# Kernel optimization log

Hardware: AMD Instinct MI355X
Metric: run time of the kernel (lower is better)

The kernel has to match this reference:

```python
import jax, jax.numpy as jnp
import numpy as np


def _gru_dir(x, Wih, Whh, bih, bhh):
    # x: (B,T,I) -> (B,T,H); torch GRU equations, h0 = 0
    H = Whh.shape[1]
    pre = x @ Wih.T + bih  # (B,T,3H), input projection hoisted out of scan
    def step(h, p):
        gh = h @ Whh.T + bhh
        pr, pz, pn = jnp.split(p, 3, axis=-1)
        gr, gz, gn = jnp.split(gh, 3, axis=-1)
        r = jax.nn.sigmoid(pr + gr)
        z = jax.nn.sigmoid(pz + gz)
        n = jnp.tanh(pn + r * gn)
        h = (1.0 - z) * n + z * h
        return h, h
    h0 = jnp.zeros((x.shape[0], H), x.dtype)
    _, ys = jax.lax.scan(step, h0, jnp.swapaxes(pre, 0, 1))
    return jnp.swapaxes(ys, 0, 1)


def _gru_bidir(x, Wih, Whh, bih, bhh):
    f = _gru_dir(x, Wih[0], Whh[0], bih[0], bhh[0])
    b = _gru_dir(x[:, ::-1], Wih[1], Whh[1], bih[1], bhh[1])[:, ::-1]
    return jnp.concatenate([f, b], axis=-1)


def _forward(inputs, embed, l_Wih, l_Whh, l_bih, l_bhh, r_Wih, r_Whh, r_bih, r_bhh,
             a_Wih, a_Whh, a_bih, a_bhh, Wc1, Wc2, vc, Wb, Wd, vd, Wm, vm, Ws, vs,
             Wp, vp, Wpred):
    x = embed[inputs]  # (B,T,E)
    hl = _gru_bidir(x, l_Wih, l_Whh, l_bih, l_bhh)  # (B,T,2H)
    hr = _gru_bidir(x, r_Wih, r_Whh, r_bih, r_bhh)  # (B,T,2H)
    # co-attention: score[b,i,j] = vc . tanh(Wc1 hl_j + Wc2 hr_i)
    s = jnp.tanh((hl @ Wc1.T)[:, None, :, :] + (hr @ Wc2.T)[:, :, None, :])  # (B,T,T,H)
    ptc = jax.nn.softmax((s @ vc.T)[..., 0], axis=-1) @ hl
    # bilinear: hr (Wb hl)^T
    sjt = jnp.einsum('bid,bjd->bij', hr, hl @ Wb.T)
    ptb = jax.nn.softmax(sjt, axis=-1) @ hl
    # multiplicative: vd . tanh(Wd (hl_j * hr_i))
    p = hl[:, None, :, :] * hr[:, :, None, :]  # (B,T,T,2H)
    ptd = jax.nn.softmax((jnp.tanh(p @ Wd.T) @ vd.T)[..., 0], axis=-1) @ hl
    # subtractive: vm . tanh(Wm (hl_j - hr_i))
    d = hl[:, None, :, :] - hr[:, :, None, :]  # (B,T,T,2H)
    ptm = jax.nn.softmax((jnp.tanh(d @ Wm.T) @ vm.T)[..., 0], axis=-1) @ hl
    # self-attention on hr: vs . tanh(Ws (hr_j * hr_i))
    ss = hr[:, None, :, :] * hr[:, :, None, :]  # (B,T,T,2H)
    pts = jax.nn.softmax((jnp.tanh(ss @ Ws.T) @ vs.T)[..., 0], axis=-1) @ hr
    agg = jnp.concatenate([hr, pts, ptc, ptd, ptb, ptm], axis=-1)  # (B,T,12H)
    ar = _gru_bidir(agg, a_Wih, a_Whh, a_bih, a_bhh)  # (B,T,2H)
    # pooling of hl
    sj = jax.nn.softmax(jnp.swapaxes(jnp.tanh(hl @ Wp.T) @ vp.T, 1, 2), axis=-1)  # (B,1,T)
    rl = sj @ hl  # (B,1,2H)
    # final attention over aggregation
    sj2 = jax.nn.softmax(jnp.swapaxes((ar @ Wc1.T + rl @ Wc2.T) @ vc.T, 1, 2), axis=-1)  # (B,1,T)
    rr = (sj2 @ ar)[:, 0, :]  # (B,2H)
    return jax.nn.sigmoid(rr @ Wpred.T)  # (B,labels)


def setup_inputs() -> dict:
    B, T, V, E, H, L = 4, 256, 30000, 300, 128, 2
    key = jax.random.key(0)
    ks = jax.random.split(key, 40)
    inp = {}
    inp['inputs'] = jax.random.randint(ks[0], (B, T), 0, V)
    inp['embed'] = jax.random.uniform(ks[1], (V, E), jnp.float32, -0.1, 0.1)
    ki = 2
    for name, isz in [('l', E), ('r', E), ('a', 12 * H)]:
        inp[name + '_Wih'] = jax.random.normal(ks[ki], (2, 3 * H, isz), jnp.float32) * 0.05; ki += 1
        inp[name + '_Whh'] = jax.random.normal(ks[ki], (2, 3 * H, H), jnp.float32) * 0.05; ki += 1
        inp[name + '_bih'] = jnp.zeros((2, 3 * H), jnp.float32)
        inp[name + '_bhh'] = jnp.zeros((2, 3 * H), jnp.float32)
    for n, o, i in [('Wc1', H, 2 * H), ('Wc2', H, 2 * H), ('vc', 1, H), ('Wb', 2 * H, 2 * H),
                    ('Wd', H, 2 * H), ('vd', 1, H), ('Wm', H, 2 * H), ('vm', 1, H),
                    ('Ws', H, 2 * H), ('vs', 1, H), ('Wp', H, 2 * H), ('vp', 1, H),
                    ('Wpred', L, 2 * H)]:
        inp[n] = jax.random.normal(ks[ki], (o, i), jnp.float32) * 0.05; ki += 1
    return inp


def reference(inputs, embed, l_Wih, l_Whh, l_bih, l_bhh, r_Wih, r_Whh, r_bih, r_bhh,
              a_Wih, a_Whh, a_bih, a_bhh, Wc1, Wc2, vc, Wb, Wd, vd, Wm, vm, Ws, vs,
              Wp, vp, Wpred):
    return _forward(inputs, embed, l_Wih, l_Whh, l_bih, l_bhh, r_Wih, r_Whh, r_bih,
                    r_bhh, a_Wih, a_Whh, a_bih, a_bhh, Wc1, Wc2, vc, Wb, Wd, vd, Wm,
                    vm, Ws, vs, Wp, vp, Wpred)
```

## Files before the change

### kernel.cpp

```cpp
#include <hip/hip_runtime.h>


#define DEV static __device__ __forceinline__
#define BAR_LGKM() __asm__ volatile("s_waitcnt lgkmcnt(0)\ns_barrier" ::: "memory")

typedef __attribute__((ext_vector_type(4))) float f32x4;
typedef __attribute__((ext_vector_type(8))) short s16x8;
typedef __attribute__((ext_vector_type(4))) unsigned int u32x4;
typedef __attribute__((ext_vector_type(2))) unsigned int u32x2;

constexpr int T = 256, E = 300, EP = 320, H = 128, H2 = 256, H3 = 384, H12 = 1536;
constexpr int M = 1024;
constexpr int STY = 262144;

DEV float b2f(unsigned short h) { return __uint_as_float(((unsigned)h) << 16); }
DEV unsigned short f2b(float f) {
  unsigned u = __float_as_uint(f);
  u += 0x7fff + ((u >> 16) & 1);
  return (unsigned short)(u >> 16);
}
DEV unsigned cvt_pk_bf16(float lo, float hi) {
  unsigned r;
  __asm__("v_cvt_pk_bf16_f32 %0, %1, %2" : "=v"(r) : "v"(lo), "v"(hi));
  return r;
}
DEV float rcp_f(float x) {
  float r;
  __asm__("v_rcp_f32 %0, %1" : "=v"(r) : "v"(x));
  return r;
}
DEV float sigm(float x) { return rcp_f(1.f + __expf(-x)); }
DEV float tanh_f(float x) {
  float e = __expf(2.f * x);
  return __builtin_fmaf(-2.f, rcp_f(e + 1.f), 1.f);
}
DEV float plsel(float x0, float x1) {
  u32x2 r = __builtin_amdgcn_permlane32_swap(
      __float_as_uint(x0), __float_as_uint(x1), false, false);
  return __uint_as_float(r[0]);
}

DEV s16x8 ldfrag(const unsigned short* p) {
  u32x4 v = *(const u32x4*)p;
  return __builtin_bit_cast(s16x8, v);
}
DEV f32x4 mfma16(s16x8 a, s16x8 b, f32x4 c) {
  return __builtin_amdgcn_mfma_f32_16x16x32_bf16(a, b, c, 0, 0, 0);
}


struct StageArgs {
  const float* cs[9]; unsigned short* cd[9]; int cn[9];
  const int* idx; const float* emb; unsigned short* xhi; unsigned short* xlo;
  const float* lW; const float* rW; unsigned short* wpad;
  int bo[12];
};

__global__ void k_stage(StageArgs sa) {
  int blk = blockIdx.x;
  int seg = 0;
  #pragma unroll
  for (int s2 = 1; s2 < 11; ++s2) seg = (blk >= sa.bo[s2]) ? s2 : seg;
  int i = (blk - sa.bo[seg]) * 256 + threadIdx.x;
  if (seg < 9) {
    if (i < sa.cn[seg]) sa.cd[seg][i] = f2b(sa.cs[seg][i]);
    return;
  }
  if (seg == 9) {
    if (i >= M * EP) return;
    int m = i / EP, e = i - m * EP;
    int r = sa.idx[m];
    float v = (e < E) ? sa.emb[(size_t)r * E + e] : 0.f;
    unsigned short hi = f2b(v);
    sa.xhi[i] = hi;
    sa.xlo[i] = f2b(v - b2f(hi));
    return;
  }
  if (i >= 4 * H3 * EP) return;
  int e = i % EP, n = (i / EP) % H3, uu = i / (EP * H3);
  const float* src = (uu < 2 ? sa.lW : sa.rW) + (size_t)((uu & 1) * H3 + n) * E;
  sa.wpad[i] = (e < E) ? f2b(src[e]) : (unsigned short)0;
}


struct GemmDesc {
  const unsigned short* Ahi; const unsigned short* Alo; const unsigned short* W;
  const float* bias; float* Cf; int N; int K; int tr;
};
struct GemmBatch { GemmDesc d[8]; };

__global__ __launch_bounds__(256) void k_gemm(GemmBatch gb) {
  GemmDesc g = gb.d[blockIdx.z];
  int nb = blockIdx.y * 64;
  if (nb >= g.N) return;
  int mb = blockIdx.x * 64;
  int lane = threadIdx.x & 63, w = threadIdx.x >> 6, quad = lane >> 4, l16 = lane & 15;
  int K = g.K;
  const unsigned short* Ahp = g.Ahi + (size_t)(mb + w * 16 + l16) * K + quad * 8;
  const unsigned short* Alp = g.Alo + (size_t)(mb + w * 16 + l16) * K + quad * 8;
  const unsigned short* Wp = g.W + (size_t)(nb + l16) * K + quad * 8;
  f32x4 acc[4];
  #pragma unroll
  for (int nt = 0; nt < 4; ++nt) acc[nt] = f32x4{0.f, 0.f, 0.f, 0.f};
  for (int k = 0; k < K; k += 32) {
    s16x8 ah = ldfrag(Ahp + k);
    s16x8 al = ldfrag(Alp + k);
    #pragma unroll
    for (int nt = 0; nt < 4; ++nt) {
      s16x8 b = ldfrag(Wp + (size_t)nt * 16 * K + k);
      acc[nt] = mfma16(ah, b, acc[nt]);
      acc[nt] = mfma16(al, b, acc[nt]);
    }
  }
  int mr0 = mb + w * 16 + quad * 4;
  #pragma unroll
  for (int nt = 0; nt < 4; ++nt) {
    int col = nb + nt * 16 + l16;
    float bv = g.bias ? g.bias[col] : 0.f;
    #pragma unroll
    for (int r = 0; r < 4; ++r) {
      if (g.tr)
        g.Cf[(size_t)col * M + (mr0 + r)] = acc[nt][r] + bv;
      else
        g.Cf[(size_t)(mr0 + r) * g.N + col] = acc[nt][r] + bv;
    }
  }
}


struct RecArgs {
  const unsigned short* whh[4];
  const float* pre[4];
  float* outf[4];
  unsigned short* outhi[4];
  unsigned short* outlo[4];
  unsigned short* agghi[4];
  unsigned short* agglo[4];
  const float* bhh[4];
  int colOff[4];
  int dir[4];
};

#define GRU_STEP(pr_, pz_, pn_, pq_, hcur_, hnxt_, s_)                         \
  {                                                                            \
    float pr = pr_, pz = pz_, pn = pn_;                                        \
    pq_ += pst2;                                                               \
    pr_ = pq_[0] + bh_r; pz_ = pq_[128] + bh_z; pn_ = pq_[256];                \
    const unsigned short* hb_ = hcur_ + l16 * 136 + quad * 8;                  \
    s16x8 ah0 = ldfrag(hb_);                                                   \
    s16x8 ah1 = ldfrag(hb_ + 32);                                              \
    s16x8 ah2 = ldfrag(hb_ + 64);                                              \
    s16x8 ah3 = ldfrag(hb_ + 96);                                              \
    f32x4 z4 = f32x4{0.f, 0.f, 0.f, 0.f};                                      \
    f32x4 aR0 = mfma16(ah0, bq[0][0], z4);                                     \
    f32x4 aR1 = mfma16(ah2, bq[0][2], z4);                                     \
    aR0 = mfma16(ah1, bq[0][1], aR0);                                          \
    aR1 = mfma16(ah3, bq[0][3], aR1);                                          \
    f32x4 aZ0 = mfma16(ah0, bq[1][0], z4);                                     \
    f32x4 aZ1 = mfma16(ah2, bq[1][2], z4);                                     \
    aZ0 = mfma16(ah1, bq[1][1], aZ0);                                          \
    aZ1 = mfma16(ah3, bq[1][3], aZ1);                                          \
    float r0 = (aR0[0] + aR1[0]) + (aR0[1] + aR1[1]);                          \
    float r1v = (aR0[2] + aR1[2]) + (aR0[3] + aR1[3]);                         \
    float rg = sigm(pr + plsel(r0, r1v));                                      \
    f32x4 aN0 = mfma16(ah0, bq[2][0], z4);                                     \
    f32x4 aN1 = mfma16(ah2, bq[2][2], z4);                                     \
    aN0 = mfma16(ah1, bq[2][1], aN0);                                          \
    aN1 = mfma16(ah3, bq[2][3], aN1);                                          \
    float z0 = (aZ0[0] + aZ1[0]) + (aZ0[1] + aZ1[1]);                          \
    float z1 = (aZ0[2] + aZ1[2]) + (aZ0[3] + aZ1[3]);                          \
    float zg = sigm(pz + plsel(z0, z1));                                       \
    float n0 = (aN0[0] + aN1[0]) + (aN0[1] + aN1[1]);                          \
    float n1 = (aN0[2] + aN1[2]) + (aN0[3] + aN1[3]);                          \
    float ng = tanh_f(pn + rg * (plsel(n0, n1) + bh_n));                       \
    hf = __builtin_fmaf(zg, hf - ng, ng);                                      \
    unsigned hp32 = cvt_pk_bf16(hf, hf);                                       \
    float rem = hf - __uint_as_float(hp32 << 16);                              \
    unsigned lp32 = cvt_pk_bf16(rem, rem);                                     \
    unsigned short hi = (unsigned short)hp32;                                  \
    unsigned short lo = (unsigned short)lp32;                                  \
    hnxt_[(2 * b) * 136 + d] = hi;                                             \
    hnxt_[(2 * b + 1) * 136 + d] = lo;                                         \
    int tq = dir ? (T - 1 - (s_)) : (s_);                                      \
    size_t o_ = (size_t)(b * T + tq) * H2 + colOff + d;                        \
    outf[o_] = hf; outhi[o_] = hi; outlo[o_] = lo;                             \
    if (agghi) {                                                               \
      size_t a_ = (size_t)(b * T + tq) * H12 + colOff + d;                     \
      agghi[a_] = hi; agglo[a_] = lo;                                          \
    }                                                                          \
    BAR_LGKM();                                                                \
  }

__global__ __launch_bounds__(512) void k_gru(RecArgs ra) {
  int u = blockIdx.x;
  __shared__ __align__(16) unsigned short hs[2][16 * 136];
  int tid = threadIdx.x, lane = tid & 63, w8 = tid >> 6;
  int quad = lane >> 4, l16 = lane & 15;
  for (int i = tid; i < 2 * 16 * 136; i += 512) ((unsigned short*)hs)[i] = 0;
  const unsigned short* whh = ra.whh[u];
  s16x8 bq[3][4];
  #pragma unroll
  for (int g = 0; g < 3; ++g) {
    int row = g * 128 + w8 * 16 + l16;
    #pragma unroll
    for (int kc = 0; kc < 4; ++kc)
      bq[g][kc] = ldfrag(whh + (size_t)row * H + kc * 32 + quad * 8);
  }
  const float* bhh = ra.bhh[u];
  const float* pre = ra.pre[u];
  float* outf = ra.outf[u];
  unsigned short* outhi = ra.outhi[u];
  unsigned short* outlo = ra.outlo[u];
  unsigned short* agghi = ra.agghi[u];
  unsigned short* agglo = ra.agglo[u];
  int colOff = ra.colOff[u], dir = ra.dir[u];
  int b = ((quad & 1) << 1) | (quad >> 1);
  int d = w8 * 16 + l16;
  float bh_r = bhh[d], bh_z = bhh[d + 128], bh_n = bhh[d + 256];
  float hf = 0.f;
  int t0 = dir ? (T - 1) : 0;
  long pst = dir ? -(long)H3 : (long)H3;
  long pst2 = 2 * pst;
  const float* pqE = pre + (size_t)(b * T + t0) * H3 + d;
  const float* pqO = pqE + pst;
  float e_pr = pqE[0] + bh_r, e_pz = pqE[128] + bh_z, e_pn = pqE[256];
  float o_pr = pqO[0] + bh_r, o_pz = pqO[128] + bh_z, o_pn = pqO[256];
  __syncthreads();
  for (int s = 0; s < T; s += 2) {
    GRU_STEP(e_pr, e_pz, e_pn, pqE, hs[0], hs[1], s);
    GRU_STEP(o_pr, o_pz, o_pn, pqO, hs[1], hs[0], s + 1);
  }
}


struct ScMMArgs {
  const unsigned short* Xhi[2];
  const float* Rf; const float* Wt[2]; const float* vt[2];
  float* So[2]; float* So2[2];
};

__global__ __launch_bounds__(256, 2) void k_scmm(ScMMArgs a) {
  __shared__ __align__(16) unsigned short w_lds[64 * 256];
  int which = blockIdx.y;
  int bi = blockIdx.x, b = bi >> 8;
  int tid = threadIdx.x;
  int type = which >> 1, khb = which & 1;
  const unsigned short* Xhi = a.Xhi[type];
  const float* W = a.Wt[type] + (size_t)khb * 64 * 256;
  const float* v = a.vt[type] + khb * 64;
  float* Sout = khb ? a.So2[type] : a.So[type];
  int lane = tid & 63, w = tid >> 6, quad = lane >> 4, l16 = lane & 15;
  int d4 = tid & 63, rhi = tid >> 6;
  float4 h4 = ((const float4*)(a.Rf + (size_t)bi * 256))[d4];
  #pragma unroll
  for (int it = 0; it < 16; ++it) {
    int kl = it * 4 + rhi;
    float4 w4 = ((const float4*)(W + (size_t)kl * 256))[d4];
    unsigned lo32 = cvt_pk_bf16(w4.x * h4.x, w4.y * h4.y);
    unsigned hi32 = cvt_pk_bf16(w4.z * h4.z, w4.w * h4.w);
    unsigned long long pk = (unsigned long long)lo32 | ((unsigned long long)hi32 << 32);
    int gphys = ((d4 >> 1) + kl) & 31;
    *(unsigned long long*)(w_lds + (size_t)kl * 256 + gphys * 8 + (d4 & 1) * 4) = pk;
  }
  BAR_LGKM();
  f32x4 acc[4][4];
  #pragma unroll
  for (int jj = 0; jj < 4; ++jj)
    #pragma unroll
    for (int c = 0; c < 4; ++c) acc[jj][c] = f32x4{0.f, 0.f, 0.f, 0.f};
  const unsigned short* Xp0 =
      Xhi + (size_t)(b * 256 + w * 4 * 16 + l16) * 256 + quad * 8;
  #pragma unroll 2
  for (int kc = 0; kc < 8; ++kc) {
    s16x8 af[4];
    #pragma unroll
    for (int c = 0; c < 4; ++c) {
      int krow = c * 16 + l16;
      int gp = (kc * 4 + quad + krow) & 31;
      af[c] = ldfrag(w_lds + (size_t)krow * 256 + gp * 8);
    }
    s16x8 bf[4];
    #pragma unroll
    for (int jj = 0; jj < 4; ++jj)
      bf[jj] = ldfrag(Xp0 + (size_t)jj * 16 * 256 + kc * 32);
    #pragma unroll
    for (int jj = 0; jj < 4; ++jj)
      #pragma unroll
      for (int c = 0; c < 4; ++c)
        acc[jj][c] = mfma16(af[c], bf[jj], acc[jj][c]);
  }
  float vv[4][4];
  #pragma unroll
  for (int c = 0; c < 4; ++c)
    #pragma unroll
    for (int r = 0; r < 4; ++r) vv[c][r] = v[c * 16 + quad * 4 + r];
  #pragma unroll
  for (int jj = 0; jj < 4; ++jj) {
    float s = 0.f;
    #pragma unroll
    for (int c = 0; c < 4; ++c)
      #pragma unroll
      for (int r = 0; r < 4; ++r) s += tanh_f(acc[jj][c][r]) * vv[c][r];
    s += __shfl_xor(s, 16);
    s += __shfl_xor(s, 32);
    int jt = w * 4 + jj;
    if (lane < 16) Sout[(size_t)bi * 256 + jt * 16 + l16] = s;
  }
}


struct ScCmbArgs {
  const float *Hc, *Rc, *Hm, *Rm, *HB, *hrf, *vcf, *vmf; float* S;
};

__global__ __launch_bounds__(256, 2) void k_sccmb(ScCmbArgs a) {
  int bi = blockIdx.x;
  int tid = threadIdx.x;
  __shared__ float rc_l[4 * 128];
  __shared__ float rm_l[4 * 128];
  __shared__ float hr_l[4 * 256];
  __shared__ float vc_l[128], vm_l[128];
  int b = bi >> 6, i0 = (bi & 63) << 2;
  int gi0 = b * 256 + i0;
  {
    const float4* hr4 = (const float4*)(a.hrf + (size_t)gi0 * 256);
    ((float4*)hr_l)[tid] = hr4[tid];
    if (tid < 128) {
      const float4* rc4 = (const float4*)(a.Rc + (size_t)gi0 * 128);
      const float4* rm4 = (const float4*)(a.Rm + (size_t)gi0 * 128);
      ((float4*)rc_l)[tid] = rc4[tid];
      ((float4*)rm_l)[tid] = rm4[tid];
      vc_l[tid] = a.vcf[tid]; vm_l[tid] = a.vmf[tid];
    }
  }
  __syncthreads();
  int j = tid;
  size_t cb = (size_t)(b * 256 + j);
  float scq[4], smq[4], sbq[4];
  #pragma unroll
  for (int q = 0; q < 4; ++q) { scq[q] = 0.f; smq[q] = 0.f; sbq[q] = 0.f; }
  for (int k = 0; k < 128; ++k) {
    float hc = a.Hc[(size_t)k * M + cb];
    float hm = a.Hm[(size_t)k * M + cb];
    float vck = vc_l[k], vmk = vm_l[k];
    #pragma unroll
    for (int q = 0; q < 4; ++q) {
      scq[q] += vck * tanh_f(hc + rc_l[q * 128 + k]);
      smq[q] += vmk * tanh_f(hm - rm_l[q * 128 + k]);
    }
  }
  for (int k = 0; k < 256; ++k) {
    float hb = a.HB[(size_t)k * M + cb];
    #pragma unroll
    for (int q = 0; q < 4; ++q) sbq[q] += hb * hr_l[q * 256 + k];
  }
  #pragma unroll
  for (int q = 0; q < 4; ++q) {
    size_t o = (size_t)(gi0 + q) * 256 + j;
    a.S[(size_t)STY * 1 + o] = scq[q];
    a.S[(size_t)STY * 3 + o] = sbq[q];
    a.S[(size_t)STY * 4 + o] = smq[q];
  }
}


__global__ __launch_bounds__(256) void k_wsum(const float* __restrict__ S,
    const float* __restrict__ S2,
    const float* __restrict__ hl_f, const float* __restrict__ hr_f,
    unsigned short* __restrict__ ahi, unsigned short* __restrict__ alo) {
  int it = blockIdx.x, type = blockIdx.y, b = blockIdx.z;
  __shared__ float p_l[8][256];
  __shared__ float red[4];
  int tid = threadIdx.x;
  for (int ii = 0; ii < 8; ++ii) {
    size_t idx = ((size_t)(b * 256 + it * 8 + ii)) * 256 + tid;
    float x = S[(size_t)type * STY + idx];
    if (type == 0) x += S2[idx];
    else if (type == 2) x += S2[(size_t)STY + idx];
    float m = x;
    for (int dl = 32; dl; dl >>= 1) m = fmaxf(m, __shfl_xor(m, dl));
    if ((tid & 63) == 0) red[tid >> 6] = m;
    __syncthreads();
    m = fmaxf(fmaxf(red[0], red[1]), fmaxf(red[2], red[3]));
    __syncthreads();
    float e = __expf(x - m);
    float sum = e;
    for (int dl = 32; dl; dl >>= 1) sum += __shfl_xor(sum, dl);
    if ((tid & 63) == 0) red[tid >> 6] = sum;
    __syncthreads();
    sum = red[0] + red[1] + red[2] + red[3];
    p_l[ii][tid] = e * rcp_f(sum);
    __syncthreads();
  }
  const float* src = (type == 0 ? hr_f : hl_f) + (size_t)b * 256 * 256;
  float acc[8] = {0.f, 0.f, 0.f, 0.f, 0.f, 0.f, 0.f, 0.f};
  for (int j = 0; j < 256; ++j) {
    float hv = src[(size_t)j * 256 + tid];
    #pragma unroll
    for (int ii = 0; ii < 8; ++ii) acc[ii] += p_l[ii][j] * hv;
  }
  int off = 256 * (1 + type);
  #pragma unroll
  for (int ii = 0; ii < 8; ++ii) {
    float vv = acc[ii];
    unsigned short hi = f2b(vv);
    size_t o = (size_t)(b * 256 + it * 8 + ii) * H12 + off + tid;
    ahi[o] = hi;
    alo[o] = f2b(vv - b2f(hi));
  }
}


__global__ __launch_bounds__(256) void k_tail(const float* __restrict__ Hp,
    const float* __restrict__ hl_f, const float* __restrict__ vpf,
    const float* __restrict__ Wc2f, const float* __restrict__ Arc,
    const float* __restrict__ ar_f, const float* __restrict__ vcf,
    const float* __restrict__ Wpredf, float* __restrict__ out) {
  int b = blockIdx.x, tid = threadIdx.x;
  __shared__ float vl[128], wl[256], rvec[256], rlcl[128], red[4];
  if (tid < 128) vl[tid] = vpf[tid];
  __syncthreads();
  const float* hp = Hp + (size_t)(b * 256 + tid) * 128;
  float s = 0.f;
  for (int k = 0; k < 128; ++k) s += vl[k] * tanh_f(hp[k]);
  float m = s;
  for (int dl = 32; dl; dl >>= 1) m = fmaxf(m, __shfl_xor(m, dl));
  if ((tid & 63) == 0) red[tid >> 6] = m;
  __syncthreads();
  m = fmaxf(fmaxf(red[0], red[1]), fmaxf(red[2], red[3]));
  __syncthreads();
  float e = __expf(s - m);
  float sum = e;
  for (int dl = 32; dl; dl >>= 1) sum += __shfl_xor(sum, dl);
  if ((tid & 63) == 0) red[tid >> 6] = sum;
  __syncthreads();
  sum = red[0] + red[1] + red[2] + red[3];
  wl[tid] = e * rcp_f(sum);
  __syncthreads();
  float acc = 0.f;
  for (int t = 0; t < 256; ++t) acc += wl[t] * hl_f[(size_t)(b * 256 + t) * 256 + tid];
  rvec[tid] = acc;
  __syncthreads();
  if (tid < 128) {
    float a2 = 0.f;
    const float* wr = Wc2f + (size_t)tid * 256;
    for (int dk = 0; dk < 256; ++dk) a2 += rvec[dk] * wr[dk];
    rlcl[tid] = a2;
    vl[tid] = vcf[tid];
  }
  __syncthreads();
  const float* ap = Arc + (size_t)(b * 256 + tid) * 128;
  float s2 = 0.f;
  for (int k = 0; k < 128; ++k) s2 += vl[k] * (ap[k] + rlcl[k]);
  m = s2;
  for (int dl = 32; dl; dl >>= 1) m = fmaxf(m, __shfl_xor(m, dl));
  if ((tid & 63) == 0) red[tid >> 6] = m;
  __syncthreads();
  m = fmaxf(fmaxf(red[0], red[1]), fmaxf(red[2], red[3]));
  __syncthreads();
  float e2 = __expf(s2 - m);
  float sum2 = e2;
  for (int dl = 32; dl; dl >>= 1) sum2 += __shfl_xor(sum2, dl);
  if ((tid & 63) == 0) red[tid >> 6] = sum2;
  __syncthreads();
  sum2 = red[0] + red[1] + red[2] + red[3];
  wl[tid] = e2 * rcp_f(sum2);
  __syncthreads();
  float acc2 = 0.f;
  for (int t = 0; t < 256; ++t) acc2 += wl[t] * ar_f[(size_t)(b * 256 + t) * 256 + tid];
  rvec[tid] = acc2;
  __syncthreads();
  if (tid < 2) {
    float o = 0.f;
    const float* wp = Wpredf + (size_t)tid * 256;
    for (int dk = 0; dk < 256; ++dk) o += rvec[dk] * wp[dk];
    out[b * 2 + tid] = sigm(o);
  }
}


extern "C" void kernel_launch(void* const* d_in, const int* in_sizes, int n_in,
                              void* d_out, int out_size, void* d_ws, size_t ws_size,
                              hipStream_t stream) {
  (void)in_sizes; (void)n_in; (void)out_size; (void)ws_size;
  const int* inputs = (const int*)d_in[0];
  const float* embed = (const float*)d_in[1];
  const float* lWih = (const float*)d_in[2];
  const float* lWhh = (const float*)d_in[3];
  const float* lbih = (const float*)d_in[4];
  const float* lbhh = (const float*)d_in[5];
  const float* rWih = (const float*)d_in[6];
  const float* rWhh = (const float*)d_in[7];
  const float* rbih = (const float*)d_in[8];
  const float* rbhh = (const float*)d_in[9];
  const float* aWih = (const float*)d_in[10];
  const float* aWhh = (const float*)d_in[11];
  const float* abih = (const float*)d_in[12];
  const float* abhh = (const float*)d_in[13];
  const float* Wc1 = (const float*)d_in[14];
  const float* Wc2 = (const float*)d_in[15];
  const float* vc  = (const float*)d_in[16];
  const float* Wb  = (const float*)d_in[17];
  const float* Wd  = (const float*)d_in[18];
  const float* vd  = (const float*)d_in[19];
  const float* Wm  = (const float*)d_in[20];
  const float* vmv = (const float*)d_in[21];
  const float* Wsw = (const float*)d_in[22];
  const float* vsv = (const float*)d_in[23];
  const float* Wp  = (const float*)d_in[24];
  const float* vp  = (const float*)d_in[25];
  const float* Wpred = (const float*)d_in[26];

  char* ws = (char*)d_ws;
  size_t off = 0;
  auto alloc = [&](size_t bytes) -> void* {
    void* p = ws + off;
    off += (bytes + 255) & ~(size_t)255;
    return p;
  };
  unsigned short* xhi = (unsigned short*)alloc((size_t)M * EP * 2);
  unsigned short* xlo = (unsigned short*)alloc((size_t)M * EP * 2);
  unsigned short* wpad = (unsigned short*)alloc((size_t)4 * H3 * EP * 2);
  unsigned short* Whh_b = (unsigned short*)alloc((size_t)6 * H3 * H * 2);
  unsigned short* aWih_b = (unsigned short*)alloc((size_t)2 * H3 * H12 * 2);
  unsigned short* Wc1_b = (unsigned short*)alloc((size_t)H * H2 * 2);
  unsigned short* Wc2_b = (unsigned short*)alloc((size_t)H * H2 * 2);
  unsigned short* Wm_b  = (unsigned short*)alloc((size_t)H * H2 * 2);
  unsigned short* Wp_b  = (unsigned short*)alloc((size_t)H * H2 * 2);
  unsigned short* Wb_b  = (unsigned short*)alloc((size_t)H2 * H2 * 2);
  char* region1 = (char*)alloc((size_t)4 * M * H3 * 4);
  float* pre_lr = (float*)region1;
  float* S      = (float*)region1;
  float* pre_a  = (float*)region1;
  float* S2 = (float*)alloc((size_t)2 * STY * 4);
  float* hl_f = (float*)alloc((size_t)M * H2 * 4);
  float* hr_f = (float*)alloc((size_t)M * H2 * 4);
  unsigned short* hl_hi = (unsigned short*)alloc((size_t)M * H2 * 2);
  unsigned short* hl_lo = (unsigned short*)alloc((size_t)M * H2 * 2);
  unsigned short* hr_hi = (unsigned short*)alloc((size_t)M * H2 * 2);
  unsigned short* hr_lo = (unsigned short*)alloc((size_t)M * H2 * 2);
  float* Hc = (float*)alloc((size_t)M * H * 4);
  float* Rc = (float*)alloc((size_t)M * H * 4);
  float* Hm = (float*)alloc((size_t)M * H * 4);
  float* Rm = (float*)alloc((size_t)M * H * 4);
  float* Hp = (float*)alloc((size_t)M * H * 4);
  float* HB = (float*)alloc((size_t)M * H2 * 4);
  unsigned short* agg_hi = (unsigned short*)alloc((size_t)M * H12 * 2);
  unsigned short* agg_lo = (unsigned short*)alloc((size_t)M * H12 * 2);
  float* ar_f = (float*)alloc((size_t)M * H2 * 4);
  unsigned short* ar_hi = (unsigned short*)alloc((size_t)M * H2 * 2);
  unsigned short* ar_lo = (unsigned short*)alloc((size_t)M * H2 * 2);
  float* Arc = (float*)alloc((size_t)M * H * 4);

  StageArgs sa{};
  sa.cs[0] = lWhh;  sa.cd[0] = Whh_b;                 sa.cn[0] = 2 * H3 * H;
  sa.cs[1] = rWhh;  sa.cd[1] = Whh_b + 2 * H3 * H;    sa.cn[1] = 2 * H3 * H;
  sa.cs[2] = aWhh;  sa.cd[2] = Whh_b + 4 * H3 * H;    sa.cn[2] = 2 * H3 * H;
  sa.cs[3] = aWih;  sa.cd[3] = aWih_b;                sa.cn[3] = 2 * H3 * H12;
  sa.cs[4] = Wc1;   sa.cd[4] = Wc1_b;                 sa.cn[4] = H * H2;
  sa.cs[5] = Wc2;   sa.cd[5] = Wc2_b;                 sa.cn[5] = H * H2;
  sa.cs[6] = Wm;    sa.cd[6] = Wm_b;                  sa.cn[6] = H * H2;
  sa.cs[7] = Wp;    sa.cd[7] = Wp_b;                  sa.cn[7] = H * H2;
  sa.cs[8] = Wb;    sa.cd[8] = Wb_b;                  sa.cn[8] = H2 * H2;
  sa.idx = inputs; sa.emb = embed; sa.xhi = xhi; sa.xlo = xlo;
  sa.lW = lWih; sa.rW = rWih; sa.wpad = wpad;
  {
    int acc0 = 0;
    sa.bo[0] = 0;
    for (int s = 0; s < 9; ++s) { acc0 += (sa.cn[s] + 255) / 256; sa.bo[s + 1] = acc0; }
    acc0 += (M * EP + 255) / 256;       sa.bo[10] = acc0;
    acc0 += (4 * H3 * EP + 255) / 256;  sa.bo[11] = acc0;
  }
  k_stage<<<dim3(sa.bo[11]), dim3(256), 0, stream>>>(sa);

  GemmBatch ga{};
  const float* biases[4] = { lbih, lbih + H3, rbih, rbih + H3 };
  for (int u = 0; u < 4; ++u)
    ga.d[u] = GemmDesc{ xhi, xlo, wpad + (size_t)u * H3 * EP, biases[u],
                        pre_lr + (size_t)u * M * H3, H3, EP, 0 };
  k_gemm<<<dim3(16, 6, 4), dim3(256), 0, stream>>>(ga);

  RecArgs r1{};
  r1.whh[0] = Whh_b;               r1.whh[1] = Whh_b + H3 * H;
  r1.whh[2] = Whh_b + 2 * H3 * H;  r1.whh[3] = Whh_b + 3 * H3 * H;
  for (int u = 0; u < 4; ++u) r1.pre[u] = pre_lr + (size_t)u * M * H3;
  r1.outf[0] = r1.outf[1] = hl_f; r1.outf[2] = r1.outf[3] = hr_f;
  r1.outhi[0] = r1.outhi[1] = hl_hi; r1.outhi[2] = r1.outhi[3] = hr_hi;
  r1.outlo[0] = r1.outlo[1] = hl_lo; r1.outlo[2] = r1.outlo[3] = hr_lo;
  r1.agghi[0] = r1.agghi[1] = nullptr; r1.agghi[2] = r1.agghi[3] = agg_hi;
  r1.agglo[0] = r1.agglo[1] = nullptr; r1.agglo[2] = r1.agglo[3] = agg_lo;
  r1.bhh[0] = lbhh; r1.bhh[1] = lbhh + H3; r1.bhh[2] = rbhh; r1.bhh[3] = rbhh + H3;
  r1.colOff[0] = 0; r1.colOff[1] = H; r1.colOff[2] = 0; r1.colOff[3] = H;
  r1.dir[0] = 0; r1.dir[1] = 1; r1.dir[2] = 0; r1.dir[3] = 1;
  k_gru<<<dim3(4), dim3(512), 0, stream>>>(r1);

  GemmBatch gbB{};
  gbB.d[0] = GemmDesc{ hl_hi, hl_lo, Wc1_b, nullptr, Hc, H, H2, 1 };
  gbB.d[1] = GemmDesc{ hr_hi, hr_lo, Wc2_b, nullptr, Rc, H, H2, 0 };
  gbB.d[2] = GemmDesc{ hl_hi, hl_lo, Wm_b, nullptr, Hm, H, H2, 1 };
  gbB.d[3] = GemmDesc{ hr_hi, hr_lo, Wm_b, nullptr, Rm, H, H2, 0 };
  gbB.d[4] = GemmDesc{ hl_hi, hl_lo, Wb_b, nullptr, HB, H2, H2, 1 };
  gbB.d[5] = GemmDesc{ hl_hi, hl_lo, Wp_b, nullptr, Hp, H, H2, 0 };
  k_gemm<<<dim3(16, 4, 6), dim3(256), 0, stream>>>(gbB);

  ScMMArgs sm{};
  sm.Xhi[0] = hl_hi; sm.Wt[0] = Wd;  sm.vt[0] = vd;  sm.So[0] = S + (size_t)2 * STY;
  sm.Xhi[1] = hr_hi; sm.Wt[1] = Wsw; sm.vt[1] = vsv; sm.So[1] = S + (size_t)0 * STY;
  sm.So2[0] = S2 + (size_t)STY;
  sm.So2[1] = S2;
  sm.Rf = hr_f;
  k_scmm<<<dim3(M, 4), dim3(256), 0, stream>>>(sm);

  ScCmbArgs scb{};
  scb.Hc = Hc; scb.Rc = Rc; scb.Hm = Hm; scb.Rm = Rm; scb.HB = HB;
  scb.hrf = hr_f; scb.vcf = vc; scb.vmf = vmv; scb.S = S;
  k_sccmb<<<dim3(256), dim3(256), 0, stream>>>(scb);

  k_wsum<<<dim3(32, 5, 4), dim3(256), 0, stream>>>(S, S2, hl_f, hr_f, agg_hi, agg_lo);

  GemmBatch gc{};
  gc.d[0] = GemmDesc{ agg_hi, agg_lo, aWih_b, abih, pre_a, H3, H12, 0 };
  gc.d[1] = GemmDesc{ agg_hi, agg_lo, aWih_b + (size_t)H3 * H12, abih + H3,
                      pre_a + (size_t)M * H3, H3, H12, 0 };
  k_gemm<<<dim3(16, 6, 2), dim3(256), 0, stream>>>(gc);

  RecArgs r2{};
  r2.whh[0] = Whh_b + 4 * H3 * H; r2.whh[1] = Whh_b + 5 * H3 * H;
  r2.whh[2] = r2.whh[3] = Whh_b + 4 * H3 * H;
  r2.pre[0] = pre_a; r2.pre[1] = pre_a + (size_t)M * H3;
  r2.pre[2] = r2.pre[3] = pre_a;
  r2.outf[0] = r2.outf[1] = r2.outf[2] = r2.outf[3] = ar_f;
  r2.outhi[0] = r2.outhi[1] = r2.outhi[2] = r2.outhi[3] = ar_hi;
  r2.outlo[0] = r2.outlo[1] = r2.outlo[2] = r2.outlo[3] = ar_lo;
  for (int u = 0; u < 4; ++u) { r2.agghi[u] = nullptr; r2.agglo[u] = nullptr; }
  r2.bhh[0] = abhh; r2.bhh[1] = abhh + H3; r2.bhh[2] = r2.bhh[3] = abhh;
  r2.colOff[0] = 0; r2.colOff[1] = H; r2.colOff[2] = r2.colOff[3] = 0;
  r2.dir[0] = 0; r2.dir[1] = 1; r2.dir[2] = r2.dir[3] = 0;
  k_gru<<<dim3(2), dim3(512), 0, stream>>>(r2);

  GemmBatch gd{};
  gd.d[0] = GemmDesc{ ar_hi, ar_lo, Wc1_b, nullptr, Arc, H, H2, 0 };
  k_gemm<<<dim3(16, 2, 1), dim3(256), 0, stream>>>(gd);

  k_tail<<<dim3(4), dim3(256), 0, stream>>>(Hp, hl_f, vp, Wc2, Arc, ar_f, vc, Wpred,
                                            (float*)d_out);
}
```

Measured before the change: 687.3 us.

## Defer GRU global stores a step and merge projection GEMMs into score kernel

The GRU step now issues the previous step's output stores after its LDS fragment loads, so global writes overlap the next step's matrix work instead of sitting right before the barrier. A final store after the loop writes out the last step. The batched projection GEMM launch is folded into the k_scmm launch as extra grid rows (y<6), and the GEMM body is factored into a device function. This removes one kernel launch and lets the GEMM and score blocks run at the same time, at the cost of many idle blocks on the GEMM rows and shared LDS sizing.

Measured after the change: 698.5 us. About the same (+1.6%).

```diff
diff --git a/kernel.cpp b/kernel.cpp
--- a/kernel.cpp
+++ b/kernel.cpp
@@ -89,12 +89,8 @@
 };
 struct GemmBatch { GemmDesc d[8]; };
 
-__global__ __launch_bounds__(256) void k_gemm(GemmBatch gb) {
-  GemmDesc g = gb.d[blockIdx.z];
-  int nb = blockIdx.y * 64;
-  if (nb >= g.N) return;
-  int mb = blockIdx.x * 64;
-  int lane = threadIdx.x & 63, w = threadIdx.x >> 6, quad = lane >> 4, l16 = lane & 15;
+DEV void gemm_body(const GemmDesc& g, int mb, int nb, int tid) {
+  int lane = tid & 63, w = tid >> 6, quad = lane >> 4, l16 = lane & 15;
   int K = g.K;
   const unsigned short* Ahp = g.Ahi + (size_t)(mb + w * 16 + l16) * K + quad * 8;
   const unsigned short* Alp = g.Alo + (size_t)(mb + w * 16 + l16) * K + quad * 8;
@@ -125,6 +121,13 @@
         g.Cf[(size_t)(mr0 + r) * g.N + col] = acc[nt][r] + bv;
     }
   }
+}
+
+__global__ __launch_bounds__(256) void k_gemm(GemmBatch gb) {
+  GemmDesc g = gb.d[blockIdx.z];
+  int nb = blockIdx.y * 64;
+  if (nb >= g.N) return;
+  gemm_body(g, blockIdx.x * 64, nb, threadIdx.x);
 }
 
 
@@ -143,14 +146,18 @@
 
 #define GRU_STEP(pr_, pz_, pn_, pq_, hcur_, hnxt_, s_)                         \
   {                                                                            \
-    float pr = pr_, pz = pz_, pn = pn_;                                        \
-    pq_ += pst2;                                                               \
-    pr_ = pq_[0] + bh_r; pz_ = pq_[128] + bh_z; pn_ = pq_[256];                \
     const unsigned short* hb_ = hcur_ + l16 * 136 + quad * 8;                  \
     s16x8 ah0 = ldfrag(hb_);                                                   \
     s16x8 ah1 = ldfrag(hb_ + 32);                                              \
     s16x8 ah2 = ldfrag(hb_ + 64);                                              \
     s16x8 ah3 = ldfrag(hb_ + 96);                                              \
+    if (s_) {                                                                  \
+      outf[p_o] = p_hf; outhi[p_o] = p_hi; outlo[p_o] = p_lo;                  \
+      if (agghi) { agghi[p_a] = p_hi; agglo[p_a] = p_lo; }                     \
+    }                                                                          \
+    float pr = pr_, pz = pz_, pn = pn_;                                        \
+    pq_ += pst2;                                                               \
+    pr_ = pq_[0] + bh_r; pz_ = pq_[128] + bh_z; pn_ = pq_[256];                \
     f32x4 z4 = f32x4{0.f, 0.f, 0.f, 0.f};                                      \
     f32x4 aR0 = mfma16(ah0, bq[0][0], z4);                                     \
     f32x4 aR1 = mfma16(ah2, bq[0][2], z4);                                     \
@@ -182,12 +189,9 @@
     hnxt_[(2 * b) * 136 + d] = hi;                                             \
     hnxt_[(2 * b + 1) * 136 + d] = lo;                                         \
     int tq = dir ? (T - 1 - (s_)) : (s_);                                      \
-    size_t o_ = (size_t)(b * T + tq) * H2 + colOff + d;                        \
-    outf[o_] = hf; outhi[o_] = hi; outlo[o_] = lo;                             \
-    if (agghi) {                                                               \
-      size_t a_ = (size_t)(b * T + tq) * H12 + colOff + d;                     \
-      agghi[a_] = hi; agglo[a_] = lo;                                          \
-    }                                                                          \
+    p_hf = hf; p_hi = hi; p_lo = lo;                                           \
+    p_o = (size_t)(b * T + tq) * H2 + colOff + d;                              \
+    p_a = (size_t)(b * T + tq) * H12 + colOff + d;                             \
     BAR_LGKM();                                                                \
   }
 
@@ -218,6 +222,9 @@
   int d = w8 * 16 + l16;
   float bh_r = bhh[d], bh_z = bhh[d + 128], bh_n = bhh[d + 256];
   float hf = 0.f;
+  float p_hf = 0.f;
+  unsigned short p_hi = 0, p_lo = 0;
+  size_t p_o = 0, p_a = 0;
   int t0 = dir ? (T - 1) : 0;
   long pst = dir ? -(long)H3 : (long)H3;
   long pst2 = 2 * pst;
@@ -230,6 +237,8 @@
     GRU_STEP(e_pr, e_pz, e_pn, pqE, hs[0], hs[1], s);
     GRU_STEP(o_pr, o_pz, o_pn, pqO, hs[1], hs[0], s + 1);
   }
+  outf[p_o] = p_hf; outhi[p_o] = p_hi; outlo[p_o] = p_lo;
+  if (agghi) { agghi[p_a] = p_hi; agglo[p_a] = p_lo; }
 }
 
 
@@ -238,12 +247,24 @@
   const float* Rf; const float* Wt[2]; const float* vt[2];
   float* So[2]; float* So2[2];
 };
-
-__global__ __launch_bounds__(256, 2) void k_scmm(ScMMArgs a) {
+struct FuseArgs { GemmDesc d[6]; ScMMArgs sm; };
+
+__global__ __launch_bounds__(256, 2) void k_fuse(FuseArgs fa) {
   __shared__ __align__(16) unsigned short w_lds[64 * 256];
-  int which = blockIdx.y;
+  int y = blockIdx.y;
+  int tid = threadIdx.x;
+  if (y < 6) {
+    int xx = blockIdx.x;
+    if (xx >= 64) return;
+    GemmDesc g = fa.d[y];
+    int nb = (xx >> 4) * 64;
+    if (nb >= g.N) return;
+    gemm_body(g, (xx & 15) * 64, nb, tid);
+    return;
+  }
+  const ScMMArgs& a = fa.sm;
+  int which = y - 6;
   int bi = blockIdx.x, b = bi >> 8;
-  int tid = threadIdx.x;
   int type = which >> 1, khb = which & 1;
   const unsigned short* Xhi = a.Xhi[type];
   const float* W = a.Wt[type] + (size_t)khb * 64 * 256;
@@ -594,22 +615,21 @@
   r1.dir[0] = 0; r1.dir[1] = 1; r1.dir[2] = 0; r1.dir[3] = 1;
   k_gru<<<dim3(4), dim3(512), 0, stream>>>(r1);
 
-  GemmBatch gbB{};
-  gbB.d[0] = GemmDesc{ hl_hi, hl_lo, Wc1_b, nullptr, Hc, H, H2, 1 };
-  gbB.d[1] = GemmDesc{ hr_hi, hr_lo, Wc2_b, nullptr, Rc, H, H2, 0 };
-  gbB.d[2] = GemmDesc{ hl_hi, hl_lo, Wm_b, nullptr, Hm, H, H2, 1 };
-  gbB.d[3] = GemmDesc{ hr_hi, hr_lo, Wm_b, nullptr, Rm, H, H2, 0 };
-  gbB.d[4] = GemmDesc{ hl_hi, hl_lo, Wb_b, nullptr, HB, H2, H2, 1 };
-  gbB.d[5] = GemmDesc{ hl_hi, hl_lo, Wp_b, nullptr, Hp, H, H2, 0 };
-  k_gemm<<<dim3(16, 4, 6), dim3(256), 0, stream>>>(gbB);
-
-  ScMMArgs sm{};
-  sm.Xhi[0] = hl_hi; sm.Wt[0] = Wd;  sm.vt[0] = vd;  sm.So[0] = S + (size_t)2 * STY;
-  sm.Xhi[1] = hr_hi; sm.Wt[1] = Wsw; sm.vt[1] = vsv; sm.So[1] = S + (size_t)0 * STY;
-  sm.So2[0] = S2 + (size_t)STY;
-  sm.So2[1] = S2;
-  sm.Rf = hr_f;
-  k_scmm<<<dim3(M, 4), dim3(256), 0, stream>>>(sm);
+  FuseArgs fu{};
+  fu.d[0] = GemmDesc{ hl_hi, hl_lo, Wc1_b, nullptr, Hc, H, H2, 1 };
+  fu.d[1] = GemmDesc{ hr_hi, hr_lo, Wc2_b, nullptr, Rc, H, H2, 0 };
+  fu.d[2] = GemmDesc{ hl_hi, hl_lo, Wm_b, nullptr, Hm, H, H2, 1 };
+  fu.d[3] = GemmDesc{ hr_hi, hr_lo, Wm_b, nullptr, Rm, H, H2, 0 };
+  fu.d[4] = GemmDesc{ hl_hi, hl_lo, Wb_b, nullptr, HB, H2, H2, 1 };
+  fu.d[5] = GemmDesc{ hl_hi, hl_lo, Wp_b, nullptr, Hp, H, H2, 0 };
+  fu.sm.Xhi[0] = hl_hi; fu.sm.Wt[0] = Wd;  fu.sm.vt[0] = vd;
+  fu.sm.So[0] = S + (size_t)2 * STY;
+  fu.sm.Xhi[1] = hr_hi; fu.sm.Wt[1] = Wsw; fu.sm.vt[1] = vsv;
+  fu.sm.So[1] = S + (size_t)0 * STY;
+  fu.sm.So2[0] = S2 + (size_t)STY;
+  fu.sm.So2[1] = S2;
+  fu.sm.Rf = hr_f;
+  k_fuse<<<dim3(M, 10), dim3(256), 0, stream>>>(fu);
 
   ScCmbArgs scb{};
   scb.Hc = Hc; scb.Rc = Rc; scb.Hm = Hm; scb.Rm = Rm; scb.HB = HB;
```
